# Kernel optimization log

Measured on AMD Instinct MI355X. Metric: run time of the kernel, lower is better.

Reference implementation:

```python
import jax, jax.numpy as jnp
import numpy as np

B = 8; IMG = 256; P = 8; IN_CH = 2
HP = IMG // P; WP = HP; L = HP * WP          # 32, 32, 1024
ENC_DIM = 768; ENC_HEADS = 12; ENC_DEPTH = 6
DEC_DIM = 512; DEC_HEADS = 8;  DEC_DEPTH = 4
NUM_REL = (2 * HP - 1) * (2 * WP - 1)        # 3969
L_VIS = L // 2                               # mask_ratio = 0.5
T_IN = P * P * IN_CH; T_OUT = P * P          # 128, 64


def _make_rel_index():
    coords = np.stack(np.meshgrid(np.arange(HP), np.arange(WP), indexing='ij')).reshape(2, -1).T
    rel = coords[:, None, :] - coords[None, :, :]
    rel[..., 0] += HP - 1
    rel[..., 1] += WP - 1
    return jnp.asarray(rel[..., 0] * (2 * WP - 1) + rel[..., 1], dtype=jnp.int32)

REL = _make_rel_index()  # (L, L) static relative-position index grid


def layernorm(x, s, b):
    m = x.mean(-1, keepdims=True)
    v = jnp.var(x, axis=-1, keepdims=True)
    return (x - m) * jax.lax.rsqrt(v + 1e-5) * s + b


def vit_block(x, p, rel, n_heads):
    ln1s, ln1b, qkvw, qkvb, bt, pw, pb, ln2s, ln2b, f1w, f1b, f2w, f2b = p
    Bx, Lx, C = x.shape
    hd = C // n_heads
    h = layernorm(x, ln1s, ln1b)
    qkv = (h @ qkvw.T + qkvb).reshape(Bx, Lx, 3, n_heads, hd).transpose(2, 0, 3, 1, 4)
    q, k, v = qkv[0], qkv[1], qkv[2]                    # (B, H, Lx, hd)
    bias = bt[rel.reshape(-1)].reshape(Lx, Lx, n_heads).transpose(2, 0, 1)  # (H, Lx, Lx)
    attn = jax.nn.softmax(jnp.einsum('bhqd,bhkd->bhqk', q, k) * (hd ** -0.5) + bias[None], axis=-1)
    o = jnp.einsum('bhqk,bhkd->bhqd', attn, v).transpose(0, 2, 1, 3).reshape(Bx, Lx, C)
    x = x + o @ pw.T + pb
    h2 = layernorm(x, ln2s, ln2b)
    return x + (jax.nn.gelu(h2 @ f1w.T + f1b, approximate=False) @ f2w.T + f2b)


def run_blocks(x, stacked, rel, n_heads):
    def body(c, p):
        return vit_block(c, p, rel, n_heads), None
    return jax.lax.scan(body, x, stacked)[0]


def patchify(x):
    Bx = x.shape[0]
    x = x.reshape(Bx, IN_CH, HP, P, WP, P).transpose(0, 2, 4, 3, 5, 1)
    return x.reshape(Bx, L, T_IN)


def unpatchify(t):
    Bx = t.shape[0]
    return t.reshape(Bx, HP, WP, P, P, 1).transpose(0, 5, 1, 3, 2, 4).reshape(Bx, 1, IMG, IMG)


def setup_inputs() -> dict:
    key = jax.random.key(0)
    ks = iter(jax.random.split(key, 64))
    def nrm(shape, std=0.02):
        return jax.random.normal(next(ks), shape, jnp.float32) * std
    inp = {}
    inp['x'] = jax.random.normal(next(ks), (B, IN_CH, IMG, IMG), jnp.float32)
    perm = jax.random.permutation(next(ks), L)
    inp['visible_idx'] = jnp.sort(perm[:L_VIS]).astype(jnp.int32)
    inp['enc_embed_w'] = nrm((ENC_DIM, T_IN))
    inp['enc_embed_b'] = jnp.zeros((ENC_DIM,), jnp.float32)
    inp['pos_enc'] = nrm((1, L, ENC_DIM))
    def blk(prefix, depth, dim, heads):
        hid = 4 * dim
        inp[prefix + 'ln1s'] = jnp.ones((depth, dim), jnp.float32)
        inp[prefix + 'ln1b'] = jnp.zeros((depth, dim), jnp.float32)
        inp[prefix + 'qkvw'] = nrm((depth, 3 * dim, dim))
        inp[prefix + 'qkvb'] = jnp.zeros((depth, 3 * dim), jnp.float32)
        inp[prefix + 'bt'] = nrm((depth, NUM_REL, heads))
        inp[prefix + 'pw'] = nrm((depth, dim, dim))
        inp[prefix + 'pb'] = jnp.zeros((depth, dim), jnp.float32)
        inp[prefix + 'ln2s'] = jnp.ones((depth, dim), jnp.float32)
        inp[prefix + 'ln2b'] = jnp.zeros((depth, dim), jnp.float32)
        inp[prefix + 'f1w'] = nrm((depth, hid, dim))
        inp[prefix + 'f1b'] = jnp.zeros((depth, hid), jnp.float32)
        inp[prefix + 'f2w'] = nrm((depth, dim, hid))
        inp[prefix + 'f2b'] = jnp.zeros((depth, dim), jnp.float32)
    blk('enc_', ENC_DEPTH, ENC_DIM, ENC_HEADS)
    blk('dec_', DEC_DEPTH, DEC_DIM, DEC_HEADS)
    inp['enc_norm_s'] = jnp.ones((ENC_DIM,), jnp.float32)
    inp['enc_norm_b'] = jnp.zeros((ENC_DIM,), jnp.float32)
    inp['dec_embed_w'] = nrm((DEC_DIM, ENC_DIM))
    inp['dec_embed_b'] = jnp.zeros((DEC_DIM,), jnp.float32)
    inp['mask_token'] = nrm((1, 1, DEC_DIM))
    inp['pos_dec'] = nrm((1, L, DEC_DIM))
    inp['dec_norm_s'] = jnp.ones((DEC_DIM,), jnp.float32)
    inp['dec_norm_b'] = jnp.zeros((DEC_DIM,), jnp.float32)
    inp['head_mu_w'] = nrm((T_OUT, DEC_DIM))
    inp['head_mu_b'] = jnp.zeros((T_OUT,), jnp.float32)
    inp['head_logvar_w'] = nrm((T_OUT, DEC_DIM))
    inp['head_logvar_b'] = jnp.zeros((T_OUT,), jnp.float32)
    return inp


def reference(x, visible_idx, enc_embed_w, enc_embed_b, pos_enc,
              enc_ln1s, enc_ln1b, enc_qkvw, enc_qkvb, enc_bt, enc_pw, enc_pb,
              enc_ln2s, enc_ln2b, enc_f1w, enc_f1b, enc_f2w, enc_f2b,
              dec_ln1s, dec_ln1b, dec_qkvw, dec_qkvb, dec_bt, dec_pw, dec_pb,
              dec_ln2s, dec_ln2b, dec_f1w, dec_f1b, dec_f2w, dec_f2b,
              enc_norm_s, enc_norm_b, dec_embed_w, dec_embed_b, mask_token, pos_dec,
              dec_norm_s, dec_norm_b, head_mu_w, head_mu_b, head_logvar_w, head_logvar_b):
    Bx = x.shape[0]
    tokens = patchify(x)                                   # (B, L, T_IN)
    mask = jnp.ones((L,), jnp.float32).at[visible_idx].set(0.0)
    mask = jnp.broadcast_to(mask[None, :], (Bx, L))        # 1 = masked
    enc = tokens @ enc_embed_w.T + enc_embed_b + pos_enc   # (B, L, ENC_DIM)
    enc_vis = enc[:, visible_idx, :]                       # (B, L_VIS, ENC_DIM)
    rel_sub = REL[visible_idx][:, visible_idx]             # (L_VIS, L_VIS)
    enc_stack = (enc_ln1s, enc_ln1b, enc_qkvw, enc_qkvb, enc_bt, enc_pw, enc_pb,
                 enc_ln2s, enc_ln2b, enc_f1w, enc_f1b, enc_f2w, enc_f2b)
    enc_vis = run_blocks(enc_vis, enc_stack, rel_sub, ENC_HEADS)
    enc_vis = layernorm(enc_vis, enc_norm_s, enc_norm_b)
    dec_vis = enc_vis @ dec_embed_w.T + dec_embed_b        # (B, L_VIS, DEC_DIM)
    dec_full = jnp.broadcast_to(mask_token, (Bx, L, DEC_DIM))
    dec_full = dec_full.at[:, visible_idx, :].set(dec_vis) + pos_dec
    dec_stack = (dec_ln1s, dec_ln1b, dec_qkvw, dec_qkvb, dec_bt, dec_pw, dec_pb,
                 dec_ln2s, dec_ln2b, dec_f1w, dec_f1b, dec_f2w, dec_f2b)
    dec_full = run_blocks(dec_full, dec_stack, REL, DEC_HEADS)
    dec_full = layernorm(dec_full, dec_norm_s, dec_norm_b)
    mu_tok = dec_full @ head_mu_w.T + head_mu_b
    lv_tok = jnp.clip(dec_full @ head_logvar_w.T + head_logvar_b, -6.0, 6.0)
    return unpatchify(mu_tok), unpatchify(lv_tok), mask
```

## Files before the change

kernel.cpp:

```cpp
#include <hip/hip_runtime.h>
#include <hip/hip_bf16.h>
#include <math.h>

#define NB 8
#define LFULL 1024
#define LVIS 512
#define NREL 3969

typedef __attribute__((ext_vector_type(8))) short s8v;
typedef __attribute__((ext_vector_type(4))) float f4v;

__device__ __forceinline__ float gelu_f(float x) {
    return 0.5f * x * (1.0f + erff(x * 0.7071067811865475f));
}
__device__ __forceinline__ short f2bf(float x) {
    __hip_bfloat16 h = __float2bfloat16(x);
    return __builtin_bit_cast(short, h);
}
__device__ __forceinline__ float bf2f(short s) {
    unsigned u = ((unsigned)(unsigned short)s) << 16;
    return __builtin_bit_cast(float, u);
}

template<int MODE, bool OUTBF, bool SPLITK>
__global__ __launch_bounds__(256)
void gemm_a16(const short* __restrict__ A, const float* __restrict__ W,
              const float* __restrict__ bias, const float* res,
              void* __restrict__ Cv, int M, int N, int K)
{
    __shared__ __align__(16) short Al[16][64][8];
    __shared__ __align__(16) short Wl[16][64][8];
    const int t  = threadIdx.x;
    const int w  = t >> 6, l = t & 63;
    const int lg = l >> 4, lr = l & 15;
    const int bm = blockIdx.y * 128, bn = blockIdx.x * 128;
    const int wm = (w & 1) * 64,  wn = (w >> 1) * 64;

    const int Kc    = K / gridDim.z;
    const int kbase = blockIdx.z * Kc;

    f4v acc[4][4];
#pragma unroll
    for (int i = 0; i < 4; ++i)
#pragma unroll
        for (int j = 0; j < 4; ++j) acc[i][j] = (f4v){0.f, 0.f, 0.f, 0.f};

    const int srow = t >> 1;
    const int kc_  = t & 1;
    const int slot = (srow >> 4) * 2 + kc_;
    const int lnb  = srow & 15;
    const short* pa = A + (size_t)(bm + srow) * K + kbase + kc_ * 32;
    const float* pw = W + (size_t)(bn + srow) * K + kbase + kc_ * 32;

    const int nk = Kc >> 6;
    s8v   ra[4];
    float4 rw[8];
#pragma unroll
    for (int j = 0; j < 4; ++j) ra[j] = *(const s8v*)(pa + j * 8);
#pragma unroll
    for (int j = 0; j < 8; ++j) rw[j] = *(const float4*)(pw + j * 4);

    for (int it = 0; it < nk; ++it) {
        s8v wb[4];
#pragma unroll
        for (int j = 0; j < 4; ++j) {
            const float4 u = rw[2 * j], v = rw[2 * j + 1];
            s8v p;
            p[0]=f2bf(u.x); p[1]=f2bf(u.y); p[2]=f2bf(u.z); p[3]=f2bf(u.w);
            p[4]=f2bf(v.x); p[5]=f2bf(v.y); p[6]=f2bf(v.z); p[7]=f2bf(v.w);
            wb[j] = p;
        }
        __syncthreads();
#pragma unroll
        for (int j = 0; j < 4; ++j) {
            *(s8v*)&Al[slot][lnb + 16 * j][0] = ra[j];
            *(s8v*)&Wl[slot][lnb + 16 * j][0] = wb[j];
        }
        __syncthreads();
        if (it + 1 < nk) {
            const int k0 = (it + 1) << 6;
#pragma unroll
            for (int j = 0; j < 4; ++j) ra[j] = *(const s8v*)(pa + k0 + j * 8);
#pragma unroll
            for (int j = 0; j < 8; ++j) rw[j] = *(const float4*)(pw + k0 + j * 4);
        }
#pragma unroll
        for (int kc = 0; kc < 2; ++kc) {
            s8v af[4], bf[4];
#pragma unroll
            for (int mi = 0; mi < 4; ++mi) af[mi] = *(const s8v*)&Al[((wm >> 4) + mi) * 2 + kc][l][0];
#pragma unroll
            for (int ni = 0; ni < 4; ++ni) bf[ni] = *(const s8v*)&Wl[((wn >> 4) + ni) * 2 + kc][l][0];
#pragma unroll
            for (int mi = 0; mi < 4; ++mi)
#pragma unroll
                for (int ni = 0; ni < 4; ++ni)
                    acc[mi][ni] = __builtin_amdgcn_mfma_f32_16x16x32_bf16(af[mi], bf[ni], acc[mi][ni], 0, 0, 0);
        }
    }

    if constexpr (SPLITK) {
        float* C = (float*)Cv;
#pragma unroll
        for (int ni = 0; ni < 4; ++ni) {
            const int col = bn + wn + ni * 16 + lr;
#pragma unroll
            for (int mi = 0; mi < 4; ++mi)
#pragma unroll
                for (int r = 0; r < 4; ++r) {
                    const int rowg = bm + wm + mi * 16 + lg * 4 + r;
                    atomicAdd(&C[(size_t)rowg * N + col], acc[mi][ni][r]);
                }
        }
    } else {
#pragma unroll
        for (int ni = 0; ni < 4; ++ni) {
            const int col = bn + wn + ni * 16 + lr;
            const float bb = bias[col];
#pragma unroll
            for (int mi = 0; mi < 4; ++mi)
#pragma unroll
                for (int r = 0; r < 4; ++r) {
                    const int rowg = bm + wm + mi * 16 + lg * 4 + r;
                    float v = acc[mi][ni][r] + bb;
                    if (MODE == 1) v += res[(size_t)rowg * N + col];
                    if (MODE == 2) v = gelu_f(v);
                    if constexpr (OUTBF) ((short*)Cv)[(size_t)rowg * N + col] = f2bf(v);
                    else                 ((float*)Cv)[(size_t)rowg * N + col] = v;
                }
        }
    }
}

__global__ void prefill_k(float* __restrict__ y, const float* __restrict__ bias,
                          int N, int n)
{
    const int id = blockIdx.x * 256 + threadIdx.x;
    if (id >= n) return;
    const int col = id - (id / N) * N;
    y[id] += bias[col];
}

template<bool HAS_IDX>
__global__ __launch_bounds__(256)
void attn_v2(const short* __restrict__ qkv, const float* __restrict__ btt,
             const int* vis, short* __restrict__ out, int Lx, int Cx)
{
    __shared__ __align__(16) short Kl[64][72];
    __shared__ __align__(16) short Vl[64][72];
    __shared__ __align__(16) short Pl[4][16][72];
    __shared__ int qpos[64];
    __shared__ int kpos[64];

    const int q0 = blockIdx.x * 64;
    const int h  = blockIdx.y, bb = blockIdx.z;
    const int t  = threadIdx.x;
    const int w  = t >> 6, l = t & 63;
    const int lg = l >> 4, lr = l & 15;
    const int C3 = 3 * Cx;
    const float* bth = btt + (size_t)h * NREL;

    s8v qa[2];
    {
        const short* src = qkv + (size_t)(bb * Lx + q0 + w * 16 + lr) * C3 + h * 64 + lg * 8;
        qa[0] = *(const s8v*)(src);
        qa[1] = *(const s8v*)(src + 32);
    }
    int qi, qj;
    if (HAS_IDX) {
        if (t < 64) qpos[t] = vis[q0 + t];
        __syncthreads();
        const int qv = qpos[w * 16 + lr];
        qi = qv >> 5; qj = qv & 31;
    } else {
        const int qv = q0 + w * 16 + lr;
        qi = qv >> 5; qj = qv & 31;
    }

    float m_run = -INFINITY, l_run = 0.0f;
    f4v o[4];
#pragma unroll
    for (int df = 0; df < 4; ++df) o[df] = (f4v){0.f, 0.f, 0.f, 0.f};

    const int nt = Lx >> 6;
    for (int kt = 0; kt < nt; ++kt) {
        __syncthreads();
        {
            const int key = t >> 2, dh = (t & 3) * 16;
            const short* src = qkv + (size_t)(bb * Lx + kt * 64 + key) * C3 + Cx + h * 64 + dh;
            *(s8v*)&Kl[key][dh]     = *(const s8v*)(src);
            *(s8v*)&Kl[key][dh + 8] = *(const s8v*)(src + 8);
        }
        {
            const int key = t & 63, dh = (t >> 6) * 16;
            const short* src = qkv + (size_t)(bb * Lx + kt * 64 + key) * C3 + 2 * Cx + h * 64 + dh;
            const s8v v0 = *(const s8v*)(src);
            const s8v v1 = *(const s8v*)(src + 8);
#pragma unroll
            for (int e = 0; e < 8; ++e) Vl[dh + e][key] = v0[e];
#pragma unroll
            for (int e = 0; e < 8; ++e) Vl[dh + 8 + e][key] = v1[e];
        }
        if (HAS_IDX && t < 64) kpos[t] = vis[kt * 64 + t];
        __syncthreads();

        f4v st[4];
#pragma unroll
        for (int f = 0; f < 4; ++f) {
            st[f] = (f4v){0.f, 0.f, 0.f, 0.f};
#pragma unroll
            for (int c = 0; c < 2; ++c) {
                s8v ka = *(const s8v*)&Kl[f * 16 + lr][c * 32 + lg * 8];
                st[f] = __builtin_amdgcn_mfma_f32_16x16x32_bf16(ka, qa[c], st[f], 0, 0, 0);
            }
        }

        float sv[16];
        if (HAS_IDX) {
#pragma unroll
            for (int f = 0; f < 4; ++f)
#pragma unroll
                for (int r = 0; r < 4; ++r) {
                    const int kv = kpos[f * 16 + lg * 4 + r];
                    const int rel = (qi - (kv >> 5) + 31) * 63 + (qj - (kv & 31) + 31);
                    sv[f * 4 + r] = st[f][r] * 0.125f + bth[rel];
                }
        } else {
#pragma unroll
            for (int f = 0; f < 4; ++f) {
                const int kbase = kt * 64 + f * 16 + lg * 4;
                const int R0 = (qi - (kbase >> 5) + 31) * 63 + (qj - (kbase & 31) + 31);
#pragma unroll
                for (int r = 0; r < 4; ++r)
                    sv[f * 4 + r] = st[f][r] * 0.125f + bth[R0 - r];
            }
        }

        float mx = sv[0];
#pragma unroll
        for (int i = 1; i < 16; ++i) mx = fmaxf(mx, sv[i]);
        mx = fmaxf(mx, __shfl_xor(mx, 16));
        mx = fmaxf(mx, __shfl_xor(mx, 32));
        const float mnew = fmaxf(m_run, mx);
        const float alpha = __expf(m_run - mnew);
        float rs = 0.0f;
#pragma unroll
        for (int i = 0; i < 16; ++i) { sv[i] = __expf(sv[i] - mnew); rs += sv[i]; }
        rs += __shfl_xor(rs, 16);
        rs += __shfl_xor(rs, 32);
        l_run = l_run * alpha + rs;
        m_run = mnew;

#pragma unroll
        for (int f = 0; f < 4; ++f) {
            short4 p4;
            p4.x = f2bf(sv[f * 4 + 0]); p4.y = f2bf(sv[f * 4 + 1]);
            p4.z = f2bf(sv[f * 4 + 2]); p4.w = f2bf(sv[f * 4 + 3]);
            *(short4*)&Pl[w][lr][f * 16 + lg * 4] = p4;
        }

        float al[4];
#pragma unroll
        for (int r = 0; r < 4; ++r) al[r] = __shfl(alpha, lg * 4 + r);
#pragma unroll
        for (int df = 0; df < 4; ++df) {
            o[df][0] *= al[0]; o[df][1] *= al[1];
            o[df][2] *= al[2]; o[df][3] *= al[3];
        }
        __syncthreads();

#pragma unroll
        for (int c = 0; c < 2; ++c) {
            s8v pa = *(const s8v*)&Pl[w][lr][c * 32 + lg * 8];
#pragma unroll
            for (int df = 0; df < 4; ++df) {
                s8v vb = *(const s8v*)&Vl[df * 16 + lr][c * 32 + lg * 8];
                o[df] = __builtin_amdgcn_mfma_f32_16x16x32_bf16(pa, vb, o[df], 0, 0, 0);
            }
        }
    }

    float il[4];
#pragma unroll
    for (int r = 0; r < 4; ++r) il[r] = 1.0f / __shfl(l_run, lg * 4 + r);
#pragma unroll
    for (int df = 0; df < 4; ++df)
#pragma unroll
        for (int r = 0; r < 4; ++r)
            out[(size_t)(bb * Lx + q0 + w * 16 + lg * 4 + r) * Cx + h * 64 + df * 16 + lr] =
                f2bf(o[df][r] * il[r]);
}

__global__ void transpose_bt_k(const float* __restrict__ bt, float* __restrict__ dst,
                               int H, int n)
{
    const int id = blockIdx.x * 256 + threadIdx.x;
    if (id >= n) return;
    const int rel = id % NREL;
    const int dh  = id / NREL;
    const int h   = dh % H;
    const int d   = dh / H;
    dst[id] = bt[((size_t)d * NREL + rel) * H + h];
}

__global__ __launch_bounds__(256)
void ln_k(const float* __restrict__ x, const float* __restrict__ g,
          const float* __restrict__ be, short* __restrict__ y, int C)
{
    const int row = blockIdx.x;
    const float* xr = x + (size_t)row * C;
    float s = 0.f, ss = 0.f;
    for (int c = threadIdx.x; c < C; c += 256) { const float v = xr[c]; s += v; ss += v * v; }
#pragma unroll
    for (int off = 1; off < 64; off <<= 1) { s += __shfl_xor(s, off); ss += __shfl_xor(ss, off); }
    __shared__ float rs[4], rss[4];
    const int w = threadIdx.x >> 6;
    if ((threadIdx.x & 63) == 0) { rs[w] = s; rss[w] = ss; }
    __syncthreads();
    s  = rs[0] + rs[1] + rs[2] + rs[3];
    ss = rss[0] + rss[1] + rss[2] + rss[3];
    const float mean = s / C;
    const float rstd = rsqrtf(ss / C - mean * mean + 1e-5f);
    short* yr = y + (size_t)row * C;
    for (int c = threadIdx.x; c < C; c += 256)
        yr[c] = f2bf((xr[c] - mean) * rstd * g[c] + be[c]);
}

__global__ void gather_tokens_k(const float* __restrict__ x, const int* __restrict__ vis,
                                short* __restrict__ tok)
{
    const int id = blockIdx.x * 256 + threadIdx.x;
    const int ti = id & 127;
    const int j  = (id >> 7) & 511;
    const int b  = id >> 16;
    const int ll = vis[j];
    const int hp = ll >> 5, wp = ll & 31;
    const int pi = ti >> 4, pj = (ti >> 1) & 7, ch = ti & 1;
    tok[id] = f2bf(x[(((size_t)(b * 2 + ch) * 256) + hp * 8 + pi) * 256 + wp * 8 + pj]);
}

__global__ void add_pos_vis_k(float* __restrict__ y, const float* __restrict__ pos,
                              const int* __restrict__ vis)
{
    const int id = blockIdx.x * 256 + threadIdx.x;
    const int c = id % 768;
    const int j = (id / 768) & 511;
    y[id] += pos[(size_t)vis[j] * 768 + c];
}

__global__ void fill_dec_k(float* __restrict__ y, const float* __restrict__ mtok,
                           const float* __restrict__ pos)
{
    const int id = blockIdx.x * 256 + threadIdx.x;
    const int c = id & 511;
    const int ll = (id >> 9) & 1023;
    y[id] = mtok[c] + pos[(ll << 9) + c];
}

__global__ void scatter_vis_k(float* __restrict__ y, const short* __restrict__ dvis,
                              const float* __restrict__ pos, const int* __restrict__ vis)
{
    const int id = blockIdx.x * 256 + threadIdx.x;
    const int c = id & 511;
    const int j = (id >> 9) & 511;
    const int b = id >> 18;
    const int ll = vis[j];
    y[(((size_t)b * 1024 + ll) << 9) + c] = bf2f(dvis[id]) + pos[(ll << 9) + c];
}

__global__ void concat_heads_k(const float* __restrict__ hmw, const float* __restrict__ hlw,
                               const float* __restrict__ hmb, const float* __restrict__ hlb,
                               float* __restrict__ hw2, float* __restrict__ hb2)
{
    const int id = blockIdx.x * 256 + threadIdx.x;
    const int col = id & 511, row = id >> 9;
    hw2[id] = row < 64 ? hmw[row * 512 + col] : hlw[(row - 64) * 512 + col];
    if (id < 128) hb2[id] = id < 64 ? hmb[id] : hlb[id - 64];
}

__global__ void unpatch2_k(const float* __restrict__ ht, float* __restrict__ out_mu,
                           float* __restrict__ out_lv)
{
    const int id = blockIdx.x * 256 + threadIdx.x;
    const int j = id & 255, i = (id >> 8) & 255, b = id >> 16;
    const int hp = i >> 3, pi = i & 7, wp = j >> 3, pj = j & 7;
    const size_t tok = (size_t)b * 1024 + hp * 32 + wp;
    const int col = pi * 8 + pj;
    out_mu[id] = ht[tok * 128 + col];
    float v = ht[tok * 128 + 64 + col];
    out_lv[id] = fminf(6.0f, fmaxf(-6.0f, v));
}

__global__ void mask_fill_k(float* m) { m[blockIdx.x * 256 + threadIdx.x] = 1.0f; }

__global__ void mask_zero_k(float* m, const int* __restrict__ vis)
{
    const int id = blockIdx.x * 256 + threadIdx.x;
    const int b = id >> 9, j = id & 511;
    m[b * 1024 + vis[j]] = 0.0f;
}

extern "C" void kernel_launch(void* const* d_in, const int* in_sizes, int n_in,
                              void* d_out, int out_size, void* d_ws, size_t ws_size,
                              hipStream_t stream)
{
    const float* x       = (const float*)d_in[0];
    const int*   vis     = (const int*  )d_in[1];
    const float* eew     = (const float*)d_in[2];
    const float* eeb     = (const float*)d_in[3];
    const float* pos_enc = (const float*)d_in[4];
    const float* e_ln1s  = (const float*)d_in[5];
    const float* e_ln1b  = (const float*)d_in[6];
    const float* e_qkvw  = (const float*)d_in[7];
    const float* e_qkvb  = (const float*)d_in[8];
    const float* e_bt    = (const float*)d_in[9];
    const float* e_pw    = (const float*)d_in[10];
    const float* e_pb    = (const float*)d_in[11];
    const float* e_ln2s  = (const float*)d_in[12];
    const float* e_ln2b  = (const float*)d_in[13];
    const float* e_f1w   = (const float*)d_in[14];
    const float* e_f1b   = (const float*)d_in[15];
    const float* e_f2w   = (const float*)d_in[16];
    const float* e_f2b   = (const float*)d_in[17];
    const float* d_ln1s  = (const float*)d_in[18];
    const float* d_ln1b  = (const float*)d_in[19];
    const float* d_qkvw  = (const float*)d_in[20];
    const float* d_qkvb  = (const float*)d_in[21];
    const float* d_bt    = (const float*)d_in[22];
    const float* d_pw    = (const float*)d_in[23];
    const float* d_pb    = (const float*)d_in[24];
    const float* d_ln2s  = (const float*)d_in[25];
    const float* d_ln2b  = (const float*)d_in[26];
    const float* d_f1w   = (const float*)d_in[27];
    const float* d_f1b   = (const float*)d_in[28];
    const float* d_f2w   = (const float*)d_in[29];
    const float* d_f2b   = (const float*)d_in[30];
    const float* en_s    = (const float*)d_in[31];
    const float* en_b    = (const float*)d_in[32];
    const float* dew     = (const float*)d_in[33];
    const float* deb     = (const float*)d_in[34];
    const float* mtok    = (const float*)d_in[35];
    const float* pos_dec = (const float*)d_in[36];
    const float* dn_s    = (const float*)d_in[37];
    const float* dn_b    = (const float*)d_in[38];
    const float* hmw     = (const float*)d_in[39];
    const float* hmb     = (const float*)d_in[40];
    const float* hlw     = (const float*)d_in[41];
    const float* hlb     = (const float*)d_in[42];
    (void)in_sizes; (void)n_in; (void)out_size; (void)ws_size;

    char* base = (char*)d_ws;
    float* bx    = (float*)(base);
    short* bh    = (short*)(base + 17u * 1024 * 1024);
    short* batt  = (short*)(base + 26u * 1024 * 1024);
    short* bbig  = (short*)(base + 35u * 1024 * 1024);
    float* ht    = (float*)(base + 69u * 1024 * 1024);
    float* hw2   = (float*)(base + 74u * 1024 * 1024);
    float* hb2   = (float*)(base + 75u * 1024 * 1024);
    float* btt_e = (float*)(base + 76u * 1024 * 1024);
    float* btt_d = (float*)(base + 78u * 1024 * 1024);

    transpose_bt_k<<<(6 * 12 * NREL + 255) / 256, 256, 0, stream>>>(e_bt, btt_e, 12, 6 * 12 * NREL);
    transpose_bt_k<<<(4 * 8 * NREL + 255) / 256, 256, 0, stream>>>(d_bt, btt_d, 8, 4 * 8 * NREL);
    concat_heads_k<<<256, 256, 0, stream>>>(hmw, hlw, hmb, hlb, hw2, hb2);

    gather_tokens_k<<<NB * LVIS * 128 / 256, 256, 0, stream>>>(x, vis, bbig);
    gemm_a16<0, false, false><<<dim3(6, 32), 256, 0, stream>>>(bbig, eew, eeb, nullptr, bx, 4096, 768, 128);
    add_pos_vis_k<<<NB * LVIS * 768 / 256, 256, 0, stream>>>(bx, pos_enc, vis);

    for (int d = 0; d < 6; ++d) {
        ln_k<<<4096, 256, 0, stream>>>(bx, e_ln1s + d * 768, e_ln1b + d * 768, bh, 768);
        gemm_a16<0, true, false><<<dim3(18, 32), 256, 0, stream>>>(bh, e_qkvw + (size_t)d * 2304 * 768,
                                                                   e_qkvb + d * 2304, nullptr, bbig, 4096, 2304, 768);
        attn_v2<true><<<dim3(8, 12, NB), 256, 0, stream>>>(bbig, btt_e + (size_t)d * 12 * NREL,
                                                           vis, batt, 512, 768);
        gemm_a16<1, false, false><<<dim3(6, 32), 256, 0, stream>>>(batt, e_pw + (size_t)d * 768 * 768,
                                                                   e_pb + d * 768, bx, bx, 4096, 768, 768);
        ln_k<<<4096, 256, 0, stream>>>(bx, e_ln2s + d * 768, e_ln2b + d * 768, bh, 768);
        gemm_a16<2, true, false><<<dim3(24, 32), 256, 0, stream>>>(bh, e_f1w + (size_t)d * 3072 * 768,
                                                                   e_f1b + d * 3072, nullptr, bbig, 4096, 3072, 768);
        prefill_k<<<4096 * 768 / 256, 256, 0, stream>>>(bx, e_f2b + d * 768, 768, 4096 * 768);
        gemm_a16<0, false, true><<<dim3(6, 32, 4), 256, 0, stream>>>(bbig, e_f2w + (size_t)d * 768 * 3072,
                                                                     nullptr, nullptr, bx, 4096, 768, 3072);
    }

    ln_k<<<4096, 256, 0, stream>>>(bx, en_s, en_b, bh, 768);
    gemm_a16<0, true, false><<<dim3(4, 32), 256, 0, stream>>>(bh, dew, deb, nullptr, batt, 4096, 512, 768);
    fill_dec_k<<<NB * LFULL * 512 / 256, 256, 0, stream>>>(bx, mtok, pos_dec);
    scatter_vis_k<<<NB * LVIS * 512 / 256, 256, 0, stream>>>(bx, batt, pos_dec, vis);

    for (int d = 0; d < 4; ++d) {
        ln_k<<<8192, 256, 0, stream>>>(bx, d_ln1s + d * 512, d_ln1b + d * 512, bh, 512);
        gemm_a16<0, true, false><<<dim3(12, 64), 256, 0, stream>>>(bh, d_qkvw + (size_t)d * 1536 * 512,
                                                                   d_qkvb + d * 1536, nullptr, bbig, 8192, 1536, 512);
        attn_v2<false><<<dim3(16, 8, NB), 256, 0, stream>>>(bbig, btt_d + (size_t)d * 8 * NREL,
                                                            nullptr, batt, 1024, 512);
        gemm_a16<1, false, false><<<dim3(4, 64), 256, 0, stream>>>(batt, d_pw + (size_t)d * 512 * 512,
                                                                   d_pb + d * 512, bx, bx, 8192, 512, 512);
        ln_k<<<8192, 256, 0, stream>>>(bx, d_ln2s + d * 512, d_ln2b + d * 512, bh, 512);
        gemm_a16<2, true, false><<<dim3(16, 64), 256, 0, stream>>>(bh, d_f1w + (size_t)d * 2048 * 512,
                                                                   d_f1b + d * 2048, nullptr, bbig, 8192, 2048, 512);
        prefill_k<<<8192 * 512 / 256, 256, 0, stream>>>(bx, d_f2b + d * 512, 512, 8192 * 512);
        gemm_a16<0, false, true><<<dim3(4, 64, 4), 256, 0, stream>>>(bbig, d_f2w + (size_t)d * 512 * 2048,
                                                                     nullptr, nullptr, bx, 8192, 512, 2048);
    }

    ln_k<<<8192, 256, 0, stream>>>(bx, dn_s, dn_b, bh, 512);
    gemm_a16<0, false, false><<<dim3(1, 64), 256, 0, stream>>>(bh, hw2, hb2, nullptr, ht, 8192, 128, 512);

    float* out = (float*)d_out;
    unpatch2_k<<<NB * 65536 / 256, 256, 0, stream>>>(ht, out, out + 524288);
    mask_fill_k<<<32, 256, 0, stream>>>(out + 1048576);
    mask_zero_k<<<16, 256, 0, stream>>>(out + 1048576, vis);
}
```

Measured before the change: 3.432 ms.

## Pre-convert weights to bf16 and use direct-to-LDS double-buffered GEMM

Adds a per-layer kernel that converts each layer's fp32 weights to bf16 once, so the GEMM no longer converts W in registers for every output tile. The GEMM is rewritten to load A and W tiles into a double-buffered LDS with global_load_lds, using one barrier per K-step of 32. Split-K with atomics and the bias prefill kernel for the second FFN GEMM are replaced by a single GEMM with a residual epilogue. The cost is extra conversion kernels and weight traffic, fewer blocks for the FFN2 GEMM, and a smaller K step per iteration.

```diff
diff --git a/kernel.cpp b/kernel.cpp
--- a/kernel.cpp
+++ b/kernel.cpp
@@ -3,8 +3,6 @@
 #include <math.h>
 
 #define NB 8
-#define LFULL 1024
-#define LVIS 512
 #define NREL 3969
 
 typedef __attribute__((ext_vector_type(8))) short s8v;
@@ -22,22 +20,25 @@
     return __builtin_bit_cast(float, u);
 }
 
-template<int MODE, bool OUTBF, bool SPLITK>
+__device__ __forceinline__ void gl_lds16(const void* g, void* l) {
+    __builtin_amdgcn_global_load_lds(
+        (const __attribute__((address_space(1))) void*)g,
+        (__attribute__((address_space(3))) void*)l, 16, 0, 0);
+}
+
+template<int MODE, bool OUTBF>
 __global__ __launch_bounds__(256)
-void gemm_a16(const short* __restrict__ A, const float* __restrict__ W,
-              const float* __restrict__ bias, const float* res,
-              void* __restrict__ Cv, int M, int N, int K)
-{
-    __shared__ __align__(16) short Al[16][64][8];
-    __shared__ __align__(16) short Wl[16][64][8];
+void gemm_v3(const short* __restrict__ A, const short* __restrict__ W,
+             const float* __restrict__ bias, const float* __restrict__ res,
+             void* __restrict__ Cv, int M, int N, int K)
+{
+    __shared__ __align__(16) short Al[2][8][64][8];
+    __shared__ __align__(16) short Wl[2][8][64][8];
     const int t  = threadIdx.x;
     const int w  = t >> 6, l = t & 63;
     const int lg = l >> 4, lr = l & 15;
     const int bm = blockIdx.y * 128, bn = blockIdx.x * 128;
-    const int wm = (w & 1) * 64,  wn = (w >> 1) * 64;
-
-    const int Kc    = K / gridDim.z;
-    const int kbase = blockIdx.z * Kc;
+    const int wm = (w & 1) * 64, wn = (w >> 1) * 64;
 
     f4v acc[4][4];
 #pragma unroll
@@ -45,100 +46,78 @@
 #pragma unroll
         for (int j = 0; j < 4; ++j) acc[i][j] = (f4v){0.f, 0.f, 0.f, 0.f};
 
-    const int srow = t >> 1;
-    const int kc_  = t & 1;
-    const int slot = (srow >> 4) * 2 + kc_;
-    const int lnb  = srow & 15;
-    const short* pa = A + (size_t)(bm + srow) * K + kbase + kc_ * 32;
-    const float* pw = W + (size_t)(bn + srow) * K + kbase + kc_ * 32;
-
-    const int nk = Kc >> 6;
-    s8v   ra[4];
-    float4 rw[8];
-#pragma unroll
-    for (int j = 0; j < 4; ++j) ra[j] = *(const s8v*)(pa + j * 8);
-#pragma unroll
-    for (int j = 0; j < 8; ++j) rw[j] = *(const float4*)(pw + j * 4);
-
-    for (int it = 0; it < nk; ++it) {
-        s8v wb[4];
-#pragma unroll
-        for (int j = 0; j < 4; ++j) {
-            const float4 u = rw[2 * j], v = rw[2 * j + 1];
-            s8v p;
-            p[0]=f2bf(u.x); p[1]=f2bf(u.y); p[2]=f2bf(u.z); p[3]=f2bf(u.w);
-            p[4]=f2bf(v.x); p[5]=f2bf(v.y); p[6]=f2bf(v.z); p[7]=f2bf(v.w);
-            wb[j] = p;
-        }
+    const short* pa0 = A + (size_t)(bm + w * 32 + lr) * K + lg * 8;
+    const short* pa1 = pa0 + (size_t)16 * K;
+    const short* pw0 = W + (size_t)(bn + w * 32 + lr) * K + lg * 8;
+    const short* pw1 = pw0 + (size_t)16 * K;
+
+    const int nt = K >> 5;
+    int cur = 0;
+    gl_lds16(pa0, &Al[0][2 * w][0][0]);
+    gl_lds16(pa1, &Al[0][2 * w + 1][0][0]);
+    gl_lds16(pw0, &Wl[0][2 * w][0][0]);
+    gl_lds16(pw1, &Wl[0][2 * w + 1][0][0]);
+    __syncthreads();
+
+    for (int ts = 0; ts < nt; ++ts) {
+        if (ts + 1 < nt) {
+            const int k0 = (ts + 1) << 5;
+            gl_lds16(pa0 + k0, &Al[cur ^ 1][2 * w][0][0]);
+            gl_lds16(pa1 + k0, &Al[cur ^ 1][2 * w + 1][0][0]);
+            gl_lds16(pw0 + k0, &Wl[cur ^ 1][2 * w][0][0]);
+            gl_lds16(pw1 + k0, &Wl[cur ^ 1][2 * w + 1][0][0]);
+        }
+        s8v af[4], bf[4];
+#pragma unroll
+        for (int mi = 0; mi < 4; ++mi) af[mi] = *(const s8v*)&Al[cur][(wm >> 4) + mi][l][0];
+#pragma unroll
+        for (int ni = 0; ni < 4; ++ni) bf[ni] = *(const s8v*)&Wl[cur][(wn >> 4) + ni][l][0];
+#pragma unroll
+        for (int mi = 0; mi < 4; ++mi)
+#pragma unroll
+            for (int ni = 0; ni < 4; ++ni)
+                acc[mi][ni] = __builtin_amdgcn_mfma_f32_16x16x32_bf16(af[mi], bf[ni], acc[mi][ni], 0, 0, 0);
         __syncthreads();
-#pragma unroll
-        for (int j = 0; j < 4; ++j) {
-            *(s8v*)&Al[slot][lnb + 16 * j][0] = ra[j];
-            *(s8v*)&Wl[slot][lnb + 16 * j][0] = wb[j];
-        }
-        __syncthreads();
-        if (it + 1 < nk) {
-            const int k0 = (it + 1) << 6;
-#pragma unroll
-            for (int j = 0; j < 4; ++j) ra[j] = *(const s8v*)(pa + k0 + j * 8);
-#pragma unroll
-            for (int j = 0; j < 8; ++j) rw[j] = *(const float4*)(pw + k0 + j * 4);
-        }
-#pragma unroll
-        for (int kc = 0; kc < 2; ++kc) {
-            s8v af[4], bf[4];
-#pragma unroll
-            for (int mi = 0; mi < 4; ++mi) af[mi] = *(const s8v*)&Al[((wm >> 4) + mi) * 2 + kc][l][0];
-#pragma unroll
-            for (int ni = 0; ni < 4; ++ni) bf[ni] = *(const s8v*)&Wl[((wn >> 4) + ni) * 2 + kc][l][0];
-#pragma unroll
-            for (int mi = 0; mi < 4; ++mi)
-#pragma unroll
-                for (int ni = 0; ni < 4; ++ni)
-                    acc[mi][ni] = __builtin_amdgcn_mfma_f32_16x16x32_bf16(af[mi], bf[ni], acc[mi][ni], 0, 0, 0);
-        }
-    }
-
-    if constexpr (SPLITK) {
-        float* C = (float*)Cv;
-#pragma unroll
-        for (int ni = 0; ni < 4; ++ni) {
-            const int col = bn + wn + ni * 16 + lr;
-#pragma unroll
-            for (int mi = 0; mi < 4; ++mi)
-#pragma unroll
-                for (int r = 0; r < 4; ++r) {
-                    const int rowg = bm + wm + mi * 16 + lg * 4 + r;
-                    atomicAdd(&C[(size_t)rowg * N + col], acc[mi][ni][r]);
-                }
-        }
-    } else {
-#pragma unroll
-        for (int ni = 0; ni < 4; ++ni) {
-            const int col = bn + wn + ni * 16 + lr;
-            const float bb = bias[col];
-#pragma unroll
-            for (int mi = 0; mi < 4; ++mi)
-#pragma unroll
-                for (int r = 0; r < 4; ++r) {
-                    const int rowg = bm + wm + mi * 16 + lg * 4 + r;
-                    float v = acc[mi][ni][r] + bb;
-                    if (MODE == 1) v += res[(size_t)rowg * N + col];
-                    if (MODE == 2) v = gelu_f(v);
-                    if constexpr (OUTBF) ((short*)Cv)[(size_t)rowg * N + col] = f2bf(v);
-                    else                 ((float*)Cv)[(size_t)rowg * N + col] = v;
-                }
-        }
-    }
-}
-
-__global__ void prefill_k(float* __restrict__ y, const float* __restrict__ bias,
-                          int N, int n)
-{
-    const int id = blockIdx.x * 256 + threadIdx.x;
-    if (id >= n) return;
-    const int col = id - (id / N) * N;
-    y[id] += bias[col];
+        cur ^= 1;
+    }
+
+#pragma unroll
+    for (int ni = 0; ni < 4; ++ni) {
+        const int col = bn + wn + ni * 16 + lr;
+        const float bb = bias[col];
+#pragma unroll
+        for (int mi = 0; mi < 4; ++mi)
+#pragma unroll
+            for (int r = 0; r < 4; ++r) {
+                const int rowg = bm + wm + mi * 16 + lg * 4 + r;
+                float v = acc[mi][ni][r] + bb;
+                if (MODE == 1) v += res[(size_t)rowg * N + col];
+                if (MODE == 2) v = gelu_f(v);
+                if constexpr (OUTBF) ((short*)Cv)[(size_t)rowg * N + col] = f2bf(v);
+                else                 ((float*)Cv)[(size_t)rowg * N + col] = v;
+            }
+    }
+}
+
+__global__ void cvt4_k(const float* __restrict__ p0, int n0,
+                       const float* __restrict__ p1, int n1,
+                       const float* __restrict__ p2, int n2,
+                       const float* __restrict__ p3, int n3,
+                       short* __restrict__ out, int total)
+{
+    int idx = (blockIdx.x * 256 + threadIdx.x) * 8;
+    if (idx >= total) return;
+    const float* src; int off = idx;
+    if (off < n0) src = p0;
+    else if ((off -= n0) < n1) src = p1;
+    else if ((off -= n1) < n2) src = p2;
+    else { off -= n2; src = p3; }
+    const float4 a = *(const float4*)(src + off);
+    const float4 b = *(const float4*)(src + off + 4);
+    s8v v;
+    v[0] = f2bf(a.x); v[1] = f2bf(a.y); v[2] = f2bf(a.z); v[3] = f2bf(a.w);
+    v[4] = f2bf(b.x); v[5] = f2bf(b.y); v[6] = f2bf(b.z); v[7] = f2bf(b.w);
+    *(s8v*)(out + idx) = v;
 }
 
 template<bool HAS_IDX>
@@ -370,11 +349,11 @@
 
 __global__ void concat_heads_k(const float* __restrict__ hmw, const float* __restrict__ hlw,
                                const float* __restrict__ hmb, const float* __restrict__ hlb,
-                               float* __restrict__ hw2, float* __restrict__ hb2)
+                               short* __restrict__ hw2, float* __restrict__ hb2)
 {
     const int id = blockIdx.x * 256 + threadIdx.x;
     const int col = id & 511, row = id >> 9;
-    hw2[id] = row < 64 ? hmw[row * 512 + col] : hlw[(row - 64) * 512 + col];
+    hw2[id] = f2bf(row < 64 ? hmw[row * 512 + col] : hlw[(row - 64) * 512 + col]);
     if (id < 128) hb2[id] = id < 64 ? hmb[id] : hlb[id - 64];
 }
 
@@ -451,62 +430,74 @@
 
     char* base = (char*)d_ws;
     float* bx    = (float*)(base);
-    short* bh    = (short*)(base + 17u * 1024 * 1024);
-    short* batt  = (short*)(base + 26u * 1024 * 1024);
-    short* bbig  = (short*)(base + 35u * 1024 * 1024);
-    float* ht    = (float*)(base + 69u * 1024 * 1024);
-    float* hw2   = (float*)(base + 74u * 1024 * 1024);
-    float* hb2   = (float*)(base + 75u * 1024 * 1024);
-    float* btt_e = (float*)(base + 76u * 1024 * 1024);
-    float* btt_d = (float*)(base + 78u * 1024 * 1024);
+    short* bh    = (short*)(base + 17ull * 1024 * 1024);
+    short* batt  = (short*)(base + 26ull * 1024 * 1024);
+    short* bbig  = (short*)(base + 35ull * 1024 * 1024);
+    short* wb    = (short*)(base + 69ull * 1024 * 1024);
+    short* wsm   = (short*)(base + 84ull * 1024 * 1024);
+    float* hb2   = (float*)(base + 86ull * 1024 * 1024);
+    float* ht    = (float*)(base + 87ull * 1024 * 1024);
+    float* btt_e = (float*)(base + 92ull * 1024 * 1024);
+    float* btt_d = (float*)(base + 94ull * 1024 * 1024);
+
+    short* eewb = wsm;
+    short* dewb = wsm + 98304;
+    short* hw2b = wsm + 491520;
 
     transpose_bt_k<<<(6 * 12 * NREL + 255) / 256, 256, 0, stream>>>(e_bt, btt_e, 12, 6 * 12 * NREL);
     transpose_bt_k<<<(4 * 8 * NREL + 255) / 256, 256, 0, stream>>>(d_bt, btt_d, 8, 4 * 8 * NREL);
-    concat_heads_k<<<256, 256, 0, stream>>>(hmw, hlw, hmb, hlb, hw2, hb2);
-
-    gather_tokens_k<<<NB * LVIS * 128 / 256, 256, 0, stream>>>(x, vis, bbig);
-    gemm_a16<0, false, false><<<dim3(6, 32), 256, 0, stream>>>(bbig, eew, eeb, nullptr, bx, 4096, 768, 128);
-    add_pos_vis_k<<<NB * LVIS * 768 / 256, 256, 0, stream>>>(bx, pos_enc, vis);
+    concat_heads_k<<<256, 256, 0, stream>>>(hmw, hlw, hmb, hlb, hw2b, hb2);
+    cvt4_k<<<240, 256, 0, stream>>>(eew, 98304, dew, 393216, eew, 0, eew, 0, wsm, 491520);
+
+    gather_tokens_k<<<NB * 512 * 128 / 256, 256, 0, stream>>>(x, vis, bbig);
+    gemm_v3<0, false><<<dim3(6, 32), 256, 0, stream>>>(bbig, eewb, eeb, nullptr, bx, 4096, 768, 128);
+    add_pos_vis_k<<<NB * 512 * 768 / 256, 256, 0, stream>>>(bx, pos_enc, vis);
 
     for (int d = 0; d < 6; ++d) {
+        cvt4_k<<<3456, 256, 0, stream>>>(e_qkvw + (size_t)d * 1769472, 1769472,
+                                         e_pw   + (size_t)d * 589824,  589824,
+                                         e_f1w  + (size_t)d * 2359296, 2359296,
+                                         e_f2w  + (size_t)d * 2359296, 2359296, wb, 7077888);
         ln_k<<<4096, 256, 0, stream>>>(bx, e_ln1s + d * 768, e_ln1b + d * 768, bh, 768);
-        gemm_a16<0, true, false><<<dim3(18, 32), 256, 0, stream>>>(bh, e_qkvw + (size_t)d * 2304 * 768,
-                                                                   e_qkvb + d * 2304, nullptr, bbig, 4096, 2304, 768);
+        gemm_v3<0, true><<<dim3(18, 32), 256, 0, stream>>>(bh, wb, e_qkvb + d * 2304,
+                                                           nullptr, bbig, 4096, 2304, 768);
         attn_v2<true><<<dim3(8, 12, NB), 256, 0, stream>>>(bbig, btt_e + (size_t)d * 12 * NREL,
                                                            vis, batt, 512, 768);
-        gemm_a16<1, false, false><<<dim3(6, 32), 256, 0, stream>>>(batt, e_pw + (size_t)d * 768 * 768,
-                                                                   e_pb + d * 768, bx, bx, 4096, 768, 768);
+        gemm_v3<1, false><<<dim3(6, 32), 256, 0, stream>>>(batt, wb + 1769472, e_pb + d * 768,
+                                                           bx, bx, 4096, 768, 768);
         ln_k<<<4096, 256, 0, stream>>>(bx, e_ln2s + d * 768, e_ln2b + d * 768, bh, 768);
-        gemm_a16<2, true, false><<<dim3(24, 32), 256, 0, stream>>>(bh, e_f1w + (size_t)d * 3072 * 768,
-                                                                   e_f1b + d * 3072, nullptr, bbig, 4096, 3072, 768);
-        prefill_k<<<4096 * 768 / 256, 256, 0, stream>>>(bx, e_f2b + d * 768, 768, 4096 * 768);
-        gemm_a16<0, false, true><<<dim3(6, 32, 4), 256, 0, stream>>>(bbig, e_f2w + (size_t)d * 768 * 3072,
-                                                                     nullptr, nullptr, bx, 4096, 768, 3072);
+        gemm_v3<2, true><<<dim3(24, 32), 256, 0, stream>>>(bh, wb + 2359296, e_f1b + d * 3072,
+                                                           nullptr, bbig, 4096, 3072, 768);
+        gemm_v3<1, false><<<dim3(6, 32), 256, 0, stream>>>(bbig, wb + 4718592, e_f2b + d * 768,
+                                                           bx, bx, 4096, 768, 3072);
     }
 
     ln_k<<<4096, 256, 0, stream>>>(bx, en_s, en_b, bh, 768);
-    gemm_a16<0, true, false><<<dim3(4, 32), 256, 0, stream>>>(bh, dew, deb, nullptr, batt, 4096, 512, 768);
-    fill_dec_k<<<NB * LFULL * 512 / 256, 256, 0, stream>>>(bx, mtok, pos_dec);
-    scatter_vis_k<<<NB * LVIS * 512 / 256, 256, 0, stream>>>(bx, batt, pos_dec, vis);
+    gemm_v3<0, true><<<dim3(4, 32), 256, 0, stream>>>(bh, dewb, deb, nullptr, batt, 4096, 512, 768);
+    fill_dec_k<<<NB * 1024 * 512 / 256, 256, 0, stream>>>(bx, mtok, pos_dec);
+    scatter_vis_k<<<NB * 512 * 512 / 256, 256, 0, stream>>>(bx, batt, pos_dec, vis);
 
     for (int d = 0; d < 4; ++d) {
+        cvt4_k<<<1536, 256, 0, stream>>>(d_qkvw + (size_t)d * 786432,  786432,
+                                         d_pw   + (size_t)d * 262144,  262144,
+                                         d_f1w  + (size_t)d * 1048576, 1048576,
+                                         d_f2w  + (size_t)d * 1048576, 1048576, wb, 3145728);
         ln_k<<<8192, 256, 0, stream>>>(bx, d_ln1s + d * 512, d_ln1b + d * 512, bh, 512);
-        gemm_a16<0, true, false><<<dim3(12, 64), 256, 0, stream>>>(bh, d_qkvw + (size_t)d * 1536 * 512,
-                                                                   d_qkvb + d * 1536, nullptr, bbig, 8192, 1536, 512);
+        gemm_v3<0, true><<<dim3(12, 64), 256, 0, stream>>>(bh, wb, d_qkvb + d * 1536,
+                                                           nullptr, bbig, 8192, 1536, 512);
         attn_v2<false><<<dim3(16, 8, NB), 256, 0, stream>>>(bbig, btt_d + (size_t)d * 8 * NREL,
                                                             nullptr, batt, 1024, 512);
-        gemm_a16<1, false, false><<<dim3(4, 64), 256, 0, stream>>>(batt, d_pw + (size_t)d * 512 * 512,
-                                                                   d_pb + d * 512, bx, bx, 8192, 512, 512);
+        gemm_v3<1, false><<<dim3(4, 64), 256, 0, stream>>>(batt, wb + 786432, d_pb + d * 512,
+                                                           bx, bx, 8192, 512, 512);
         ln_k<<<8192, 256, 0, stream>>>(bx, d_ln2s + d * 512, d_ln2b + d * 512, bh, 512);
-        gemm_a16<2, true, false><<<dim3(16, 64), 256, 0, stream>>>(bh, d_f1w + (size_t)d * 2048 * 512,
-                                                                   d_f1b + d * 2048, nullptr, bbig, 8192, 2048, 512);
-        prefill_k<<<8192 * 512 / 256, 256, 0, stream>>>(bx, d_f2b + d * 512, 512, 8192 * 512);
-        gemm_a16<0, false, true><<<dim3(4, 64, 4), 256, 0, stream>>>(bbig, d_f2w + (size_t)d * 512 * 2048,
-                                                                     nullptr, nullptr, bx, 8192, 512, 2048);
+        gemm_v3<2, true><<<dim3(16, 64), 256, 0, stream>>>(bh, wb + 1048576, d_f1b + d * 2048,
+                                                           nullptr, bbig, 8192, 2048, 512);
+        gemm_v3<1, false><<<dim3(4, 64), 256, 0, stream>>>(bbig, wb + 2097152, d_f2b + d * 512,
+                                                           bx, bx, 8192, 512, 2048);
     }
 
     ln_k<<<8192, 256, 0, stream>>>(bx, dn_s, dn_b, bh, 512);
-    gemm_a16<0, false, false><<<dim3(1, 64), 256, 0, stream>>>(bh, hw2, hb2, nullptr, ht, 8192, 128, 512);
+    gemm_v3<0, false><<<dim3(1, 64), 256, 0, stream>>>(bh, hw2b, hb2, nullptr, ht, 8192, 128, 512);
 
     float* out = (float*)d_out;
     unpatch2_k<<<NB * 65536 / 256, 256, 0, stream>>>(ht, out, out + 524288);
```

New measurement: 2.923 ms. 1.17x faster.
